# Kernel optimization log

Measured on AMD Instinct MI355X. Metric: run time of the kernel, lower is better.

Reference implementation:

```python
import jax, jax.numpy as jnp
import numpy as np

N = 1048576            # batch of query points
D = 3                  # n_in
N_LEVELS = 16
F_PER_LEVEL = 2
LOG2_T = 19
T = 1 << LOG2_T        # hash table size per level
MIN_RES = 16
MAX_RES = 512

# instant-NGP spatial hash primes (first prime = 1)
_PRIMES = np.array([1, 2654435761, 805459861], dtype=np.uint32)
# 2^D corner offsets of the interpolation cell, [8, D]
_OFFSETS = np.stack(np.meshgrid(*([np.arange(2)] * D), indexing='ij'), -1).reshape(-1, D).astype(np.float32)


def _resolutions():
    # geometric progression of grid resolutions between min and max
    b = np.exp((np.log(MAX_RES) - np.log(MIN_RES)) / (N_LEVELS - 1))
    return np.floor(MIN_RES * b ** np.arange(N_LEVELS)).astype(np.float32)


def setup_inputs() -> dict:
    key = jax.random.key(0)
    k1, k2 = jax.random.split(key)
    inp = jax.random.uniform(k1, (N, D), dtype=jnp.float32)  # inside bbox [0,1]^3
    params = jax.random.normal(k2, (N_LEVELS, T, F_PER_LEVEL), dtype=jnp.float32)
    return {"input": inp, "parameters": params}


def _hash_corners(ci):
    # ci: int32 [n, 8, D] integer grid coords -> int32 [n, 8] table index
    c = ci.astype(jnp.uint32)
    h = c[..., 0] * jnp.uint32(int(_PRIMES[0]))
    for d in range(1, D):
        h = h ^ (c[..., d] * jnp.uint32(int(_PRIMES[d])))
    return (h % jnp.uint32(T)).astype(jnp.int32)


def _encode(inp, parameters):
    # bbox min = 0, size = 1 -> normalized coords are the inputs themselves
    u = jnp.clip(inp, 0.0, 1.0)                       # [N, D]
    offs = jnp.asarray(_OFFSETS)                      # [8, D]
    offs_i = offs.astype(jnp.int32)
    res = jnp.asarray(_resolutions())                 # [L]

    def level(carry, xs):
        table_l, r = xs                               # [T, F], scalar
        pos = u * r                                   # [N, D]
        f = jnp.floor(pos)
        w = pos - f                                   # fractional part [N, D]
        ci = f.astype(jnp.int32)[:, None, :] + offs_i[None]   # [N, 8, D]
        idx = _hash_corners(ci)                       # [N, 8]
        feats = table_l[idx]                          # gather -> [N, 8, F]
        # multilinear interpolation weights: prod_d (w_d or 1-w_d)
        wts = jnp.prod(jnp.where(offs[None] > 0, w[:, None, :], 1.0 - w[:, None, :]), axis=-1)  # [N, 8]
        out_l = jnp.einsum('ncf,nc->nf', feats, wts)  # [N, F]
        return carry, out_l

    _, outs = jax.lax.scan(level, None, (parameters, res))    # [L, N, F]
    # combination_mode = "concat": [N, L*F]
    return jnp.transpose(outs, (1, 0, 2)).reshape(u.shape[0], N_LEVELS * F_PER_LEVEL)


def reference(input, parameters):
    return _encode(input, parameters)
```

## Files before the change

### kernel.cpp

```cpp
#include <hip/hip_runtime.h>
#include <cmath>
#include <cstdint>


constexpr uint32_t kLog2T = 19;
constexpr uint32_t kMask  = (1u << kLog2T) - 1u;
constexpr uint32_t kP1    = 2654435761u;
constexpr uint32_t kP2    = 805459861u;
constexpr uint32_t kN     = 1u << 20;
constexpr uint32_t kL     = 16;
constexpr uint32_t kBins  = 4096;

typedef float v2f __attribute__((ext_vector_type(2)));
typedef float v4f __attribute__((ext_vector_type(4)));
typedef uint32_t v4u __attribute__((ext_vector_type(4)));

__device__ __forceinline__ v2f sel_half(v4f q, uint32_t hi) {
    v2f lo; lo.x = q.x; lo.y = q.y;
    v2f h2; h2.x = q.z; h2.y = q.w;
    return hi ? h2 : lo;
}

__device__ __forceinline__ uint32_t cell_key(float x, float y, float z) {
    uint32_t qx = (uint32_t)(x * 16.0f); qx = qx > 15u ? 15u : qx;
    uint32_t qy = (uint32_t)(y * 16.0f); qy = qy > 15u ? 15u : qy;
    uint32_t qz = (uint32_t)(z * 16.0f); qz = qz > 15u ? 15u : qz;
    return (qz << 8) | (qy << 4) | qx;
}


__global__ __launch_bounds__(1024) void ngp_hist_kernel(
    const float* __restrict__ inp, uint32_t* __restrict__ bins)
{
    __shared__ uint32_t h[kBins];
    const uint32_t t = threadIdx.x;
    for (uint32_t i = t; i < kBins; i += 1024u) h[i] = 0u;
    __syncthreads();
    const uint32_t base = blockIdx.x * 1024u * 16u;
    #pragma unroll 4
    for (uint32_t k = 0; k < 16u; ++k) {
        const uint32_t n = base + k * 1024u + t;
        float x = fminf(fmaxf(inp[n * 3u + 0u], 0.0f), 1.0f);
        float y = fminf(fmaxf(inp[n * 3u + 1u], 0.0f), 1.0f);
        float z = fminf(fmaxf(inp[n * 3u + 2u], 0.0f), 1.0f);
        atomicAdd(&h[cell_key(x, y, z)], 1u);
    }
    __syncthreads();
    for (uint32_t i = t; i < kBins; i += 1024u)
        if (h[i]) atomicAdd(&bins[i], h[i]);
}

__global__ __launch_bounds__(64) void ngp_scan_kernel(
    const uint32_t* __restrict__ bins, uint32_t* __restrict__ cursor)
{
    const uint32_t t = threadIdx.x;
    uint32_t s = 0u;
    for (uint32_t i = 0; i < 64u; ++i) s += bins[t * 64u + i];
    uint32_t pre = s;
    for (int d = 1; d < 64; d <<= 1) {
        uint32_t u = __shfl_up(pre, d);
        if ((int)t >= d) pre += u;
    }
    pre -= s;
    for (uint32_t i = 0; i < 64u; ++i) {
        cursor[t * 64u + i] = pre;
        pre += bins[t * 64u + i];
    }
}

__global__ __launch_bounds__(256) void ngp_scatter_kernel(
    const float* __restrict__ inp, uint32_t* __restrict__ cursor,
    v4f* __restrict__ sorted)
{
    const uint32_t n = blockIdx.x * 256u + threadIdx.x;
    float x = fminf(fmaxf(inp[n * 3u + 0u], 0.0f), 1.0f);
    float y = fminf(fmaxf(inp[n * 3u + 1u], 0.0f), 1.0f);
    float z = fminf(fmaxf(inp[n * 3u + 2u], 0.0f), 1.0f);
    const uint32_t key = cell_key(x, y, z);
    const uint32_t pos = atomicAdd(&cursor[key], 1u);
    v4f s; s.x = x; s.y = y; s.z = z; s.w = __uint_as_float(n);
    sorted[pos] = s;
}


template <uint32_t BASE>
__global__ __launch_bounds__(256) void ngp_encode_sorted_kernel(
    const v4f* __restrict__ sorted,
    const v4f* __restrict__ tbl4,
    v2f* __restrict__ wsres,
    unsigned long long pk0, unsigned long long pk1,
    unsigned long long pk2, unsigned long long pk3)
{
    const uint32_t b = blockIdx.x;
    const uint32_t l = BASE + (b >> 12);
    const uint32_t j = ((b & 4095u) << 8) + threadIdx.x;

    unsigned long long pk = (l < 8u) ? ((l < 4u) ? pk0 : pk1)
                                     : ((l < 12u) ? pk2 : pk3);
    const float r = (float)((uint32_t)(pk >> ((l & 3u) * 16u)) & 0xFFFFu);

    const v4f s = sorted[j];
    const float px = s.x * r, py = s.y * r, pz = s.z * r;
    const float fx = floorf(px), fy = floorf(py), fz = floorf(pz);
    const float wx = px - fx, wy = py - fy, wz = pz - fz;

    const uint32_t xi  = (uint32_t)(int)fx;
    const uint32_t xi1 = xi + 1u;
    const uint32_t yi  = (uint32_t)(int)fy;
    const uint32_t zi  = (uint32_t)(int)fz;

    const uint32_t hy0 = yi * kP1, hy1 = hy0 + kP1;
    const uint32_t hz0 = zi * kP2, hz1 = hz0 + kP2;
    const uint32_t hyz00 = hy0 ^ hz0, hyz01 = hy0 ^ hz1;
    const uint32_t hyz10 = hy1 ^ hz0, hyz11 = hy1 ^ hz1;

    const uint32_t i000 = (xi  ^ hyz00) & kMask, i100 = (xi1 ^ hyz00) & kMask;
    const uint32_t i001 = (xi  ^ hyz01) & kMask, i101 = (xi1 ^ hyz01) & kMask;
    const uint32_t i010 = (xi  ^ hyz10) & kMask, i110 = (xi1 ^ hyz10) & kMask;
    const uint32_t i011 = (xi  ^ hyz11) & kMask, i111 = (xi1 ^ hyz11) & kMask;

    const uint64_t ba = (uint64_t)((const char*)tbl4 + ((size_t)l << 22));
    v4u srd;
    srd.x = (uint32_t)ba;
    srd.y = (uint32_t)(ba >> 32);
    srd.z = 0xFFFFFFFFu;
    srd.w = 0x00020000u;

    const uint32_t o00 = (i000 & ~1u) << 3, o01 = (i001 & ~1u) << 3;
    const uint32_t o10 = (i010 & ~1u) << 3, o11 = (i011 & ~1u) << 3;

    v4f q00, q01, q10, q11;
    asm volatile(
        "buffer_load_dwordx4 %0, %4, %8, 0 offen sc0\n\t"
        "buffer_load_dwordx4 %1, %5, %8, 0 offen sc0\n\t"
        "buffer_load_dwordx4 %2, %6, %8, 0 offen sc0\n\t"
        "buffer_load_dwordx4 %3, %7, %8, 0 offen sc0\n\t"
        "s_waitcnt vmcnt(0)"
        : "=&v"(q00), "=&v"(q01), "=&v"(q10), "=&v"(q11)
        : "v"(o00), "v"(o01), "v"(o10), "v"(o11), "s"(srd));

    v2f f000 = sel_half(q00, i000 & 1u), f100 = sel_half(q00, (i000 & 1u) ^ 1u);
    v2f f001 = sel_half(q01, i001 & 1u), f101 = sel_half(q01, (i001 & 1u) ^ 1u);
    v2f f010 = sel_half(q10, i010 & 1u), f110 = sel_half(q10, (i010 & 1u) ^ 1u);
    v2f f011 = sel_half(q11, i011 & 1u), f111 = sel_half(q11, (i011 & 1u) ^ 1u);

    if (xi & 1u) {
        const uint32_t p00 = i100 << 3, p01 = i101 << 3;
        const uint32_t p10 = i110 << 3, p11 = i111 << 3;
        v2f g00, g01, g10, g11;
        asm volatile(
            "buffer_load_dwordx2 %0, %4, %8, 0 offen sc0\n\t"
            "buffer_load_dwordx2 %1, %5, %8, 0 offen sc0\n\t"
            "buffer_load_dwordx2 %2, %6, %8, 0 offen sc0\n\t"
            "buffer_load_dwordx2 %3, %7, %8, 0 offen sc0\n\t"
            "s_waitcnt vmcnt(0)"
            : "=&v"(g00), "=&v"(g01), "=&v"(g10), "=&v"(g11)
            : "v"(p00), "v"(p01), "v"(p10), "v"(p11), "s"(srd));
        f100 = g00; f101 = g01; f110 = g10; f111 = g11;
    }

    const float wx1w = wx, wx0w = 1.0f - wx;
    const float wy1w = wy, wy0w = 1.0f - wy;
    const float wz1w = wz, wz0w = 1.0f - wz;
    const float wyz00w = wy0w * wz0w, wyz01w = wy0w * wz1w;
    const float wyz10w = wy1w * wz0w, wyz11w = wy1w * wz1w;

    float acc0 = 0.0f, acc1 = 0.0f;
#define NGP_ACC(F, W)                         \
    acc0 = fmaf((W), (F).x, acc0);            \
    acc1 = fmaf((W), (F).y, acc1);
    NGP_ACC(f000, wx0w * wyz00w) NGP_ACC(f100, wx1w * wyz00w)
    NGP_ACC(f001, wx0w * wyz01w) NGP_ACC(f101, wx1w * wyz01w)
    NGP_ACC(f010, wx0w * wyz10w) NGP_ACC(f110, wx1w * wyz10w)
    NGP_ACC(f011, wx0w * wyz11w) NGP_ACC(f111, wx1w * wyz11w)
#undef NGP_ACC

    v2f res; res.x = acc0; res.y = acc1;
    __builtin_nontemporal_store(res, wsres + (l - BASE) * kN + j);
}

template <uint32_t BASE>
__global__ __launch_bounds__(256) void ngp_untrans_kernel(
    const v4f* __restrict__ ws4,
    const v4f* __restrict__ sorted,
    v4f* __restrict__ out4)
{
    __shared__ v4f tile4[8][65];
    const uint32_t t  = threadIdx.x;
    const uint32_t j0 = blockIdx.x * 128u;

    #pragma unroll
    for (uint32_t it = 0; it < 2; ++it) {
        const uint32_t lo = it * 4u + (t >> 6);
        const uint32_t pc = t & 63u;
        tile4[lo][pc] = ws4[lo * (kN / 2u) + (j0 >> 1) + pc];
    }
    __syncthreads();

    const v2f* tv = (const v2f*)&tile4[0][0];
    #pragma unroll
    for (uint32_t it = 0; it < 2; ++it) {
        const uint32_t p  = it * 64u + (t >> 2);
        const uint32_t lp = t & 3u;
        const v2f a = tv[(2u * lp + 0u) * 130u + p];
        const v2f b = tv[(2u * lp + 1u) * 130u + p];
        v4f o; o.x = a.x; o.y = a.y; o.z = b.x; o.w = b.y;
        const uint32_t orig = __float_as_uint(sorted[j0 + p].w);
        __builtin_nontemporal_store(o, out4 + orig * 8u + (BASE / 2u) + lp);
    }
}


__global__ __launch_bounds__(256) void ngp_encode_direct_kernel(
    const float* __restrict__ inp, const v4f* __restrict__ tbl4,
    v2f* __restrict__ dst,
    unsigned long long pk0, unsigned long long pk1,
    unsigned long long pk2, unsigned long long pk3)
{
    const uint32_t b = blockIdx.x;
    const uint32_t l = b >> 12;
    const uint32_t n = ((b & 4095u) << 8) + threadIdx.x;
    unsigned long long pk = (l < 8u) ? ((l < 4u) ? pk0 : pk1)
                                     : ((l < 12u) ? pk2 : pk3);
    const float r = (float)((uint32_t)(pk >> ((l & 3u) * 16u)) & 0xFFFFu);
    float x = fminf(fmaxf(inp[n * 3u + 0u], 0.0f), 1.0f);
    float y = fminf(fmaxf(inp[n * 3u + 1u], 0.0f), 1.0f);
    float z = fminf(fmaxf(inp[n * 3u + 2u], 0.0f), 1.0f);
    const float px = x * r, py = y * r, pz = z * r;
    const float fx = floorf(px), fy = floorf(py), fz = floorf(pz);
    const float wx = px - fx, wy = py - fy, wz = pz - fz;
    const uint32_t xi = (uint32_t)(int)fx, yi = (uint32_t)(int)fy, zi = (uint32_t)(int)fz;
    const uint32_t hy0 = yi * kP1, hy1 = hy0 + kP1;
    const uint32_t hz0 = zi * kP2, hz1 = hz0 + kP2;
    const v2f* tbl2 = (const v2f*)tbl4;
    const uint32_t lb2 = l << kLog2T;
    float acc0 = 0.0f, acc1 = 0.0f;
#define NGP_C(HX, HY, HZ, W)                                        \
    {                                                               \
        uint32_t h = ((HX) ^ (HY) ^ (HZ)) & kMask;                  \
        v2f f = tbl2[lb2 + h];                                      \
        acc0 = fmaf((W), f.x, acc0); acc1 = fmaf((W), f.y, acc1);   \
    }
    const float wxa = 1.0f - wx, wya = 1.0f - wy, wza = 1.0f - wz;
    NGP_C(xi,      hy0, hz0, wxa * wya * wza) NGP_C(xi + 1u, hy0, hz0, wx * wya * wza)
    NGP_C(xi,      hy0, hz1, wxa * wya * wz ) NGP_C(xi + 1u, hy0, hz1, wx * wya * wz )
    NGP_C(xi,      hy1, hz0, wxa * wy  * wza) NGP_C(xi + 1u, hy1, hz0, wx * wy  * wza)
    NGP_C(xi,      hy1, hz1, wxa * wy  * wz ) NGP_C(xi + 1u, hy1, hz1, wx * wy  * wz )
#undef NGP_C
    v2f res; res.x = acc0; res.y = acc1;
    dst[n * kL + l] = res;
}

extern "C" void kernel_launch(void* const* d_in, const int* in_sizes, int n_in,
                              void* d_out, int out_size, void* d_ws, size_t ws_size,
                              hipStream_t stream)
{
    const float* inp = (const float*)d_in[0];
    const v4f* tbl4  = (const v4f*)d_in[1];

    double b = std::exp((std::log(512.0) - std::log(16.0)) / 15.0);
    unsigned long long pk[4] = {0ull, 0ull, 0ull, 0ull};
    for (int k = 0; k < 16; ++k) {
        double v;
        if (k == 0)      v = 1.0;
        else if (k == 1) v = b;
        else if (k == 2) v = b * b;
        else             v = std::pow(b, (double)k);
        unsigned long long ri = (unsigned long long)std::floor(16.0 * v);
        pk[k >> 2] |= (ri & 0xFFFFull) << ((k & 3) * 16);
    }

    const size_t offSorted = 0;
    const size_t offBins   = (size_t)16 * 1024 * 1024;
    const size_t offCursor = offBins + kBins * sizeof(uint32_t);
    const size_t offRes    = offBins + 65536;
    const size_t need      = offRes + (size_t)8 * kN * sizeof(v2f);

    if (ws_size >= need) {
        char* w = (char*)d_ws;
        v4f*      sorted = (v4f*)(w + offSorted);
        uint32_t* bins   = (uint32_t*)(w + offBins);
        uint32_t* cursor = (uint32_t*)(w + offCursor);
        v2f*      wsres  = (v2f*)(w + offRes);

        hipMemsetAsync(bins, 0, kBins * sizeof(uint32_t), stream);
        hipLaunchKernelGGL(ngp_hist_kernel, dim3(64), dim3(1024), 0, stream, inp, bins);
        hipLaunchKernelGGL(ngp_scan_kernel, dim3(1), dim3(64), 0, stream, bins, cursor);
        hipLaunchKernelGGL(ngp_scatter_kernel, dim3(kN / 256u), dim3(256), 0, stream,
                           inp, cursor, sorted);

        hipLaunchKernelGGL((ngp_encode_sorted_kernel<0>), dim3(32768), dim3(256), 0, stream,
                           sorted, tbl4, wsres, pk[0], pk[1], pk[2], pk[3]);
        hipLaunchKernelGGL((ngp_untrans_kernel<0>), dim3(kN / 128u), dim3(256), 0, stream,
                           (const v4f*)wsres, sorted, (v4f*)d_out);
        hipLaunchKernelGGL((ngp_encode_sorted_kernel<8>), dim3(32768), dim3(256), 0, stream,
                           sorted, tbl4, wsres, pk[0], pk[1], pk[2], pk[3]);
        hipLaunchKernelGGL((ngp_untrans_kernel<8>), dim3(kN / 128u), dim3(256), 0, stream,
                           (const v4f*)wsres, sorted, (v4f*)d_out);
    } else {
        hipLaunchKernelGGL(ngp_encode_direct_kernel, dim3((kN * kL) / 256u), dim3(256), 0, stream,
                           inp, tbl4, (v2f*)d_out, pk[0], pk[1], pk[2], pk[3]);
    }
}
```

Measured before the change: 555.3 us.

## Fuse per-level encode and untranspose into one eight-level-per-thread kernel

```diff
diff --git a/kernel.cpp b/kernel.cpp
--- a/kernel.cpp
+++ b/kernel.cpp
@@ -13,7 +13,6 @@
 
 typedef float v2f __attribute__((ext_vector_type(2)));
 typedef float v4f __attribute__((ext_vector_type(4)));
-typedef uint32_t v4u __attribute__((ext_vector_type(4)));
 
 __device__ __forceinline__ v2f sel_half(v4f q, uint32_t hi) {
     v2f lo; lo.x = q.x; lo.y = q.y;
@@ -84,135 +83,96 @@
 
 
 template <uint32_t BASE>
-__global__ __launch_bounds__(256) void ngp_encode_sorted_kernel(
+__global__ __launch_bounds__(256) void ngp_encode8_kernel(
     const v4f* __restrict__ sorted,
-    const v4f* __restrict__ tbl4,
-    v2f* __restrict__ wsres,
+    const v2f* __restrict__ tbl2,
+    v4f* __restrict__ out4,
     unsigned long long pk0, unsigned long long pk1,
     unsigned long long pk2, unsigned long long pk3)
 {
-    const uint32_t b = blockIdx.x;
-    const uint32_t l = BASE + (b >> 12);
-    const uint32_t j = ((b & 4095u) << 8) + threadIdx.x;
-
-    unsigned long long pk = (l < 8u) ? ((l < 4u) ? pk0 : pk1)
-                                     : ((l < 12u) ? pk2 : pk3);
-    const float r = (float)((uint32_t)(pk >> ((l & 3u) * 16u)) & 0xFFFFu);
-
+    const uint32_t j = blockIdx.x * 256u + threadIdx.x;
     const v4f s = sorted[j];
-    const float px = s.x * r, py = s.y * r, pz = s.z * r;
-    const float fx = floorf(px), fy = floorf(py), fz = floorf(pz);
-    const float wx = px - fx, wy = py - fy, wz = pz - fz;
-
-    const uint32_t xi  = (uint32_t)(int)fx;
-    const uint32_t xi1 = xi + 1u;
-    const uint32_t yi  = (uint32_t)(int)fy;
-    const uint32_t zi  = (uint32_t)(int)fz;
-
-    const uint32_t hy0 = yi * kP1, hy1 = hy0 + kP1;
-    const uint32_t hz0 = zi * kP2, hz1 = hz0 + kP2;
-    const uint32_t hyz00 = hy0 ^ hz0, hyz01 = hy0 ^ hz1;
-    const uint32_t hyz10 = hy1 ^ hz0, hyz11 = hy1 ^ hz1;
-
-    const uint32_t i000 = (xi  ^ hyz00) & kMask, i100 = (xi1 ^ hyz00) & kMask;
-    const uint32_t i001 = (xi  ^ hyz01) & kMask, i101 = (xi1 ^ hyz01) & kMask;
-    const uint32_t i010 = (xi  ^ hyz10) & kMask, i110 = (xi1 ^ hyz10) & kMask;
-    const uint32_t i011 = (xi  ^ hyz11) & kMask, i111 = (xi1 ^ hyz11) & kMask;
-
-    const uint64_t ba = (uint64_t)((const char*)tbl4 + ((size_t)l << 22));
-    v4u srd;
-    srd.x = (uint32_t)ba;
-    srd.y = (uint32_t)(ba >> 32);
-    srd.z = 0xFFFFFFFFu;
-    srd.w = 0x00020000u;
-
-    const uint32_t o00 = (i000 & ~1u) << 3, o01 = (i001 & ~1u) << 3;
-    const uint32_t o10 = (i010 & ~1u) << 3, o11 = (i011 & ~1u) << 3;
-
-    v4f q00, q01, q10, q11;
-    asm volatile(
-        "buffer_load_dwordx4 %0, %4, %8, 0 offen sc0\n\t"
-        "buffer_load_dwordx4 %1, %5, %8, 0 offen sc0\n\t"
-        "buffer_load_dwordx4 %2, %6, %8, 0 offen sc0\n\t"
-        "buffer_load_dwordx4 %3, %7, %8, 0 offen sc0\n\t"
-        "s_waitcnt vmcnt(0)"
-        : "=&v"(q00), "=&v"(q01), "=&v"(q10), "=&v"(q11)
-        : "v"(o00), "v"(o01), "v"(o10), "v"(o11), "s"(srd));
-
-    v2f f000 = sel_half(q00, i000 & 1u), f100 = sel_half(q00, (i000 & 1u) ^ 1u);
-    v2f f001 = sel_half(q01, i001 & 1u), f101 = sel_half(q01, (i001 & 1u) ^ 1u);
-    v2f f010 = sel_half(q10, i010 & 1u), f110 = sel_half(q10, (i010 & 1u) ^ 1u);
-    v2f f011 = sel_half(q11, i011 & 1u), f111 = sel_half(q11, (i011 & 1u) ^ 1u);
-
-    if (xi & 1u) {
-        const uint32_t p00 = i100 << 3, p01 = i101 << 3;
-        const uint32_t p10 = i110 << 3, p11 = i111 << 3;
-        v2f g00, g01, g10, g11;
-        asm volatile(
-            "buffer_load_dwordx2 %0, %4, %8, 0 offen sc0\n\t"
-            "buffer_load_dwordx2 %1, %5, %8, 0 offen sc0\n\t"
-            "buffer_load_dwordx2 %2, %6, %8, 0 offen sc0\n\t"
-            "buffer_load_dwordx2 %3, %7, %8, 0 offen sc0\n\t"
-            "s_waitcnt vmcnt(0)"
-            : "=&v"(g00), "=&v"(g01), "=&v"(g10), "=&v"(g11)
-            : "v"(p00), "v"(p01), "v"(p10), "v"(p11), "s"(srd));
-        f100 = g00; f101 = g01; f110 = g10; f111 = g11;
-    }
-
-    const float wx1w = wx, wx0w = 1.0f - wx;
-    const float wy1w = wy, wy0w = 1.0f - wy;
-    const float wz1w = wz, wz0w = 1.0f - wz;
-    const float wyz00w = wy0w * wz0w, wyz01w = wy0w * wz1w;
-    const float wyz10w = wy1w * wz0w, wyz11w = wy1w * wz1w;
-
-    float acc0 = 0.0f, acc1 = 0.0f;
+    const uint32_t orig = __float_as_uint(s.w);
+
+    v2f acc[8];
+
+    #pragma unroll
+    for (uint32_t i = 0; i < 8u; ++i) {
+        const uint32_t l = BASE + i;
+        const unsigned long long pk = (l < 8u) ? ((l < 4u) ? pk0 : pk1)
+                                               : ((l < 12u) ? pk2 : pk3);
+        const float r = (float)((uint32_t)(pk >> ((l & 3u) * 16u)) & 0xFFFFu);
+
+        const float px = s.x * r, py = s.y * r, pz = s.z * r;
+        const float fx = floorf(px), fy = floorf(py), fz = floorf(pz);
+        const float wx = px - fx, wy = py - fy, wz = pz - fz;
+
+        const uint32_t xi  = (uint32_t)(int)fx;
+        const uint32_t xi1 = xi + 1u;
+        const uint32_t yi  = (uint32_t)(int)fy;
+        const uint32_t zi  = (uint32_t)(int)fz;
+
+        const uint32_t hy0 = yi * kP1, hy1 = hy0 + kP1;
+        const uint32_t hz0 = zi * kP2, hz1 = hz0 + kP2;
+        const uint32_t hyz00 = hy0 ^ hz0, hyz01 = hy0 ^ hz1;
+        const uint32_t hyz10 = hy1 ^ hz0, hyz11 = hy1 ^ hz1;
+
+        const uint32_t i000 = (xi  ^ hyz00) & kMask, i100 = (xi1 ^ hyz00) & kMask;
+        const uint32_t i001 = (xi  ^ hyz01) & kMask, i101 = (xi1 ^ hyz01) & kMask;
+        const uint32_t i010 = (xi  ^ hyz10) & kMask, i110 = (xi1 ^ hyz10) & kMask;
+        const uint32_t i011 = (xi  ^ hyz11) & kMask, i111 = (xi1 ^ hyz11) & kMask;
+
+        const v2f* tl2 = tbl2 + ((size_t)l << kLog2T);
+        const v4f* tl4 = (const v4f*)tl2;
+
+        const v4f q00 = tl4[i000 >> 1];
+        const v4f q01 = tl4[i001 >> 1];
+        const v4f q10 = tl4[i010 >> 1];
+        const v4f q11 = tl4[i011 >> 1];
+
+        v2f f000 = sel_half(q00, i000 & 1u), f100 = sel_half(q00, (i000 & 1u) ^ 1u);
+        v2f f001 = sel_half(q01, i001 & 1u), f101 = sel_half(q01, (i001 & 1u) ^ 1u);
+        v2f f010 = sel_half(q10, i010 & 1u), f110 = sel_half(q10, (i010 & 1u) ^ 1u);
+        v2f f011 = sel_half(q11, i011 & 1u), f111 = sel_half(q11, (i011 & 1u) ^ 1u);
+
+        if (xi & 1u) {
+            f100 = tl2[i100];
+            f101 = tl2[i101];
+            f110 = tl2[i110];
+            f111 = tl2[i111];
+        }
+
+        const float wx1w = wx, wx0w = 1.0f - wx;
+        const float wy1w = wy, wy0w = 1.0f - wy;
+        const float wz1w = wz, wz0w = 1.0f - wz;
+        const float wyz00w = wy0w * wz0w, wyz01w = wy0w * wz1w;
+        const float wyz10w = wy1w * wz0w, wyz11w = wy1w * wz1w;
+
+        float acc0 = 0.0f, acc1 = 0.0f;
 #define NGP_ACC(F, W)                         \
-    acc0 = fmaf((W), (F).x, acc0);            \
-    acc1 = fmaf((W), (F).y, acc1);
-    NGP_ACC(f000, wx0w * wyz00w) NGP_ACC(f100, wx1w * wyz00w)
-    NGP_ACC(f001, wx0w * wyz01w) NGP_ACC(f101, wx1w * wyz01w)
-    NGP_ACC(f010, wx0w * wyz10w) NGP_ACC(f110, wx1w * wyz10w)
-    NGP_ACC(f011, wx0w * wyz11w) NGP_ACC(f111, wx1w * wyz11w)
+        acc0 = fmaf((W), (F).x, acc0);        \
+        acc1 = fmaf((W), (F).y, acc1);
+        NGP_ACC(f000, wx0w * wyz00w) NGP_ACC(f100, wx1w * wyz00w)
+        NGP_ACC(f001, wx0w * wyz01w) NGP_ACC(f101, wx1w * wyz01w)
+        NGP_ACC(f010, wx0w * wyz10w) NGP_ACC(f110, wx1w * wyz10w)
+        NGP_ACC(f011, wx0w * wyz11w) NGP_ACC(f111, wx1w * wyz11w)
 #undef NGP_ACC
-
-    v2f res; res.x = acc0; res.y = acc1;
-    __builtin_nontemporal_store(res, wsres + (l - BASE) * kN + j);
-}
-
-template <uint32_t BASE>
-__global__ __launch_bounds__(256) void ngp_untrans_kernel(
-    const v4f* __restrict__ ws4,
-    const v4f* __restrict__ sorted,
-    v4f* __restrict__ out4)
-{
-    __shared__ v4f tile4[8][65];
-    const uint32_t t  = threadIdx.x;
-    const uint32_t j0 = blockIdx.x * 128u;
+        acc[i].x = acc0;
+        acc[i].y = acc1;
+    }
 
     #pragma unroll
-    for (uint32_t it = 0; it < 2; ++it) {
-        const uint32_t lo = it * 4u + (t >> 6);
-        const uint32_t pc = t & 63u;
-        tile4[lo][pc] = ws4[lo * (kN / 2u) + (j0 >> 1) + pc];
-    }
-    __syncthreads();
-
-    const v2f* tv = (const v2f*)&tile4[0][0];
-    #pragma unroll
-    for (uint32_t it = 0; it < 2; ++it) {
-        const uint32_t p  = it * 64u + (t >> 2);
-        const uint32_t lp = t & 3u;
-        const v2f a = tv[(2u * lp + 0u) * 130u + p];
-        const v2f b = tv[(2u * lp + 1u) * 130u + p];
-        v4f o; o.x = a.x; o.y = a.y; o.z = b.x; o.w = b.y;
-        const uint32_t orig = __float_as_uint(sorted[j0 + p].w);
-        __builtin_nontemporal_store(o, out4 + orig * 8u + (BASE / 2u) + lp);
+    for (uint32_t k = 0; k < 4u; ++k) {
+        v4f o;
+        o.x = acc[2u * k].x;     o.y = acc[2u * k].y;
+        o.z = acc[2u * k + 1].x; o.w = acc[2u * k + 1].y;
+        __builtin_nontemporal_store(o, out4 + orig * 8u + (BASE / 2u) + k);
     }
 }
 
 
 __global__ __launch_bounds__(256) void ngp_encode_direct_kernel(
-    const float* __restrict__ inp, const v4f* __restrict__ tbl4,
+    const float* __restrict__ inp, const v2f* __restrict__ tbl2,
     v2f* __restrict__ dst,
     unsigned long long pk0, unsigned long long pk1,
     unsigned long long pk2, unsigned long long pk3)
@@ -232,7 +192,6 @@
     const uint32_t xi = (uint32_t)(int)fx, yi = (uint32_t)(int)fy, zi = (uint32_t)(int)fz;
     const uint32_t hy0 = yi * kP1, hy1 = hy0 + kP1;
     const uint32_t hz0 = zi * kP2, hz1 = hz0 + kP2;
-    const v2f* tbl2 = (const v2f*)tbl4;
     const uint32_t lb2 = l << kLog2T;
     float acc0 = 0.0f, acc1 = 0.0f;
 #define NGP_C(HX, HY, HZ, W)                                        \
@@ -256,7 +215,7 @@
                               hipStream_t stream)
 {
     const float* inp = (const float*)d_in[0];
-    const v4f* tbl4  = (const v4f*)d_in[1];
+    const v2f* tbl2  = (const v2f*)d_in[1];
 
     double b = std::exp((std::log(512.0) - std::log(16.0)) / 15.0);
     unsigned long long pk[4] = {0ull, 0ull, 0ull, 0ull};
@@ -271,17 +230,15 @@
     }
 
     const size_t offSorted = 0;
-    const size_t offBins   = (size_t)16 * 1024 * 1024;
+    const size_t offBins   = (size_t)kN * sizeof(v4f);
     const size_t offCursor = offBins + kBins * sizeof(uint32_t);
-    const size_t offRes    = offBins + 65536;
-    const size_t need      = offRes + (size_t)8 * kN * sizeof(v2f);
+    const size_t need      = offCursor + kBins * sizeof(uint32_t);
 
     if (ws_size >= need) {
         char* w = (char*)d_ws;
         v4f*      sorted = (v4f*)(w + offSorted);
         uint32_t* bins   = (uint32_t*)(w + offBins);
         uint32_t* cursor = (uint32_t*)(w + offCursor);
-        v2f*      wsres  = (v2f*)(w + offRes);
 
         hipMemsetAsync(bins, 0, kBins * sizeof(uint32_t), stream);
         hipLaunchKernelGGL(ngp_hist_kernel, dim3(64), dim3(1024), 0, stream, inp, bins);
@@ -289,16 +246,12 @@
         hipLaunchKernelGGL(ngp_scatter_kernel, dim3(kN / 256u), dim3(256), 0, stream,
                            inp, cursor, sorted);
 
-        hipLaunchKernelGGL((ngp_encode_sorted_kernel<0>), dim3(32768), dim3(256), 0, stream,
-                           sorted, tbl4, wsres, pk[0], pk[1], pk[2], pk[3]);
-        hipLaunchKernelGGL((ngp_untrans_kernel<0>), dim3(kN / 128u), dim3(256), 0, stream,
-                           (const v4f*)wsres, sorted, (v4f*)d_out);
-        hipLaunchKernelGGL((ngp_encode_sorted_kernel<8>), dim3(32768), dim3(256), 0, stream,
-                           sorted, tbl4, wsres, pk[0], pk[1], pk[2], pk[3]);
-        hipLaunchKernelGGL((ngp_untrans_kernel<8>), dim3(kN / 128u), dim3(256), 0, stream,
-                           (const v4f*)wsres, sorted, (v4f*)d_out);
+        hipLaunchKernelGGL((ngp_encode8_kernel<0>), dim3(kN / 256u), dim3(256), 0, stream,
+                           sorted, tbl2, (v4f*)d_out, pk[0], pk[1], pk[2], pk[3]);
+        hipLaunchKernelGGL((ngp_encode8_kernel<8>), dim3(kN / 256u), dim3(256), 0, stream,
+                           sorted, tbl2, (v4f*)d_out, pk[0], pk[1], pk[2], pk[3]);
     } else {
         hipLaunchKernelGGL(ngp_encode_direct_kernel, dim3((kN * kL) / 256u), dim3(256), 0, stream,
-                           inp, tbl4, (v2f*)d_out, pk[0], pk[1], pk[2], pk[3]);
-    }
-}
+                           inp, tbl2, (v2f*)d_out, pk[0], pk[1], pk[2], pk[3]);
+    }
+}
```

Result: slower. 713.5 us (+28.5%).
